# Kernel tuning notes

Hardware: AMD Instinct MI355X
Metric: run time of the kernel (lower is better)

The kernel has to match this reference:

```python
import jax, jax.numpy as jnp
import numpy as np

EPS = 0.0  # GINConv eps

def _gin_conv(x, edge_index, W1, b1, W2, b2, n_nodes):
    # GINConv: mlp((1+eps)*x + sum_{j in N(i)} x_j)
    src, dst = edge_index[0], edge_index[1]
    agg = jax.ops.segment_sum(x[src], dst, num_segments=n_nodes)  # [N, d]
    h = (1.0 + EPS) * x + agg
    h = jax.nn.relu(h @ W1 + b1)  # Linear -> Identity(BN off) -> ReLU
    return h @ W2 + b2            # second Linear


def setup_inputs() -> dict:
    key = jax.random.key(0)
    ks = jax.random.split(key, 10)
    N, E = 50000, 600000
    d_in, d_hid, d_out = 128, 256, 128
    x = jax.random.normal(ks[0], (N, d_in), dtype=jnp.float32)
    edge_index = jax.random.randint(ks[1], (2, E), 0, N, dtype=jnp.int64)

    def lin(k, fan_in, fan_out):
        bound = 1.0 / np.sqrt(fan_in)
        kw, kb = jax.random.split(k)
        W = jax.random.uniform(kw, (fan_in, fan_out), jnp.float32, -bound, bound)
        b = jax.random.uniform(kb, (fan_out,), jnp.float32, -bound, bound)
        return W, b

    W1a, b1a = lin(ks[2], d_in, d_hid)   # conv0 mlp: 128->256
    W2a, b2a = lin(ks[3], d_hid, d_hid)  # conv0 mlp: 256->256
    W1b, b1b = lin(ks[4], d_hid, d_hid)  # conv1 mlp: 256->256
    W2b, b2b = lin(ks[5], d_hid, d_out)  # conv1 mlp: 256->128
    return {"x": x, "W1a": W1a, "b1a": b1a, "W2a": W2a, "b2a": b2a,
            "W1b": W1b, "b1b": b1b, "W2b": W2b, "b2b": b2b,
            "edge_index": edge_index}


def reference(x, W1a, b1a, W2a, b2a, W1b, b1b, W2b, b2b, edge_index):
    n_nodes = x.shape[0]
    # layer 0: GINConv -> relu (use_bn=False; dropout is identity in eval)
    h = _gin_conv(x, edge_index, W1a, b1a, W2a, b2a, n_nodes)
    h = jax.nn.relu(h)
    # final GINConv (no activation after, per forward())
    return _gin_conv(h, edge_index, W1b, b1b, W2b, b2b, n_nodes)
```

## Files before the change

kernel.cpp:

```cpp
#include <hip/hip_runtime.h>


typedef __bf16 bf16x8 __attribute__((ext_vector_type(8)));
typedef float f32x4 __attribute__((ext_vector_type(4)));
typedef unsigned short u16x8 __attribute__((ext_vector_type(8)));
typedef unsigned short u16x4 __attribute__((ext_vector_type(4)));
typedef unsigned int uint32;

__device__ __forceinline__ unsigned short f2bf(float f) {
  uint32 u = __builtin_bit_cast(uint32, f);
  u += 0x7FFFu + ((u >> 16) & 1u);
  return (unsigned short)(u >> 16);
}
__device__ __forceinline__ float bf2f(unsigned short h) {
  return __builtin_bit_cast(float, (uint32)h << 16);
}

#define G2L16(gp, lp)                                                        \
  __builtin_amdgcn_global_load_lds(                                          \
      (const __attribute__((address_space(1))) void*)(gp),                   \
      (__attribute__((address_space(3))) void*)(lp), 16, 0, 0)

__global__ void hist(const int* __restrict__ eidx, int* __restrict__ deg, int E) {
  int e = blockIdx.x * blockDim.x + threadIdx.x;
  if (e < E) atomicAdd(&deg[eidx[e + E]], 1);
}

__global__ __launch_bounds__(256) void block_sums(const int* __restrict__ deg,
                                                  int* __restrict__ bsum, int Nn) {
  __shared__ int sm[256];
  int t = threadIdx.x;
  int i = blockIdx.x * 256 + t;
  sm[t] = (i < Nn) ? deg[i] : 0;
  __syncthreads();
#pragma unroll
  for (int off = 128; off > 0; off >>= 1) {
    if (t < off) sm[t] += sm[t + off];
    __syncthreads();
  }
  if (t == 0) bsum[blockIdx.x] = sm[0];
}

__global__ __launch_bounds__(256) void scan_bsums(int* __restrict__ bsum, int nb) {
  __shared__ int sm[256];
  int t = threadIdx.x;
  int v = (t < nb) ? bsum[t] : 0;
  sm[t] = v;
  __syncthreads();
#pragma unroll
  for (int off = 1; off < 256; off <<= 1) {
    int add = (t >= off) ? sm[t - off] : 0;
    __syncthreads();
    sm[t] += add;
    __syncthreads();
  }
  if (t < nb) bsum[t] = sm[t] - v;
}

__global__ __launch_bounds__(256) void block_scan(const int* __restrict__ deg,
                                                  const int* __restrict__ bsum,
                                                  int* __restrict__ offs,
                                                  int* __restrict__ pos, int Nn) {
  __shared__ int sm[256];
  int t = threadIdx.x;
  int i = blockIdx.x * 256 + t;
  int v = (i < Nn) ? deg[i] : 0;
  sm[t] = v;
  __syncthreads();
#pragma unroll
  for (int off = 1; off < 256; off <<= 1) {
    int add = (t >= off) ? sm[t - off] : 0;
    __syncthreads();
    sm[t] += add;
    __syncthreads();
  }
  int ex = bsum[blockIdx.x] + sm[t] - v;
  if (i < Nn) {
    offs[i] = ex;
    pos[i] = ex;
    if (i == Nn - 1) offs[Nn] = ex + v;
  }
}

__global__ void fill_csr(const int* __restrict__ eidx, int* __restrict__ pos,
                         int* __restrict__ esrc, int E) {
  int e = blockIdx.x * blockDim.x + threadIdx.x;
  if (e < E) {
    int s = eidx[e];
    int d = eidx[e + E];
    int p = atomicAdd(&pos[d], 1);
    esrc[p] = s;
  }
}

__global__ __launch_bounds__(256) void prep(
    int* __restrict__ deg, int Nn,
    const float* __restrict__ x, unsigned short* __restrict__ xb, long long n4,
    const float* __restrict__ W1a, const float* __restrict__ W2a,
    const float* __restrict__ W1b, const float* __restrict__ W2b,
    unsigned short* __restrict__ w1t, unsigned short* __restrict__ w2t,
    unsigned short* __restrict__ w3t, unsigned short* __restrict__ w4t) {
  int zb = (Nn + 255) >> 8;
  int b = blockIdx.x;
  int t = threadIdx.x;
  if (b < zb) {
    int i = b * 256 + t;
    if (i < Nn) deg[i] = 0;
  } else if (b < zb + 768) {
    int i = (b - zb) * 256 + t;
    const float* W;
    unsigned short* WT;
    int K, N, j;
    if (i < 32768) {
      W = W1a; WT = w1t; K = 128; N = 256; j = i;
    } else if (i < 98304) {
      W = W2a; WT = w2t; K = 256; N = 256; j = i - 32768;
    } else if (i < 163840) {
      W = W1b; WT = w3t; K = 256; N = 256; j = i - 98304;
    } else {
      W = W2b; WT = w4t; K = 256; N = 128; j = i - 163840;
    }
    int k = j / N, n = j - k * N;
    WT[n * K + k] = f2bf(W[j]);
  } else {
    long long i = (long long)(b - zb - 768) * 256 + t;
    long long stride = (long long)(gridDim.x - zb - 768) * 256;
    for (; i < n4; i += stride) {
      float4 v = ((const float4*)x)[i];
      u16x4 o;
      o.x = f2bf(v.x); o.y = f2bf(v.y); o.z = f2bf(v.z); o.w = f2bf(v.w);
      ((u16x4*)xb)[i] = o;
    }
  }
}

__global__ __launch_bounds__(256) void agg_bf16_128(
    unsigned short* __restrict__ out, const unsigned short* __restrict__ xb,
    const int* __restrict__ offs, const int* __restrict__ esrc, int Nn) {
  int node = blockIdx.x * 4 + (threadIdx.x >> 6);
  if (node >= Nn) return;
  int lane = threadIdx.x & 63;
  int sub = lane >> 4, l16 = lane & 15;
  int beg = offs[node], end = offs[node + 1];
  int total = end - beg + 1;
  const unsigned short* xp = xb + l16 * 8;
  float acc[8] = {};
  for (int j0 = 0; j0 < total; j0 += 16) {
#pragma unroll
    for (int u = 0; u < 4; ++u) {
      int j = j0 + u * 4 + sub;
      int rv = esrc[beg + j - (j > 0)];
      long long row = (j > 0 && j < total) ? rv : node;
      float sel = (j < total) ? 1.f : 0.f;
      u16x8 v = *(const u16x8*)(xp + row * 128);
#pragma unroll
      for (int k = 0; k < 8; ++k)
        acc[k] = fmaf(bf2f(v[k]), sel, acc[k]);
    }
  }
#pragma unroll
  for (int k = 0; k < 8; ++k) acc[k] += __shfl_xor(acc[k], 16);
#pragma unroll
  for (int k = 0; k < 8; ++k) acc[k] += __shfl_xor(acc[k], 32);
  if (sub == 0) {
    u16x8 o;
#pragma unroll
    for (int k = 0; k < 8; ++k) o[k] = f2bf(acc[k]);
    *(u16x8*)(out + (long long)node * 128 + l16 * 8) = o;
  }
}

__global__ __launch_bounds__(256) void agg_bf16_256(
    unsigned short* __restrict__ out, const unsigned short* __restrict__ h,
    const int* __restrict__ offs, const int* __restrict__ esrc, int Nn) {
  int node = blockIdx.x * 4 + (threadIdx.x >> 6);
  if (node >= Nn) return;
  int lane = threadIdx.x & 63;
  int sub = lane >> 5, l32 = lane & 31;
  int beg = offs[node], end = offs[node + 1];
  int total = end - beg + 1;
  const unsigned short* hp = h + l32 * 8;
  float acc[8] = {};
  for (int j0 = 0; j0 < total; j0 += 16) {
#pragma unroll
    for (int u = 0; u < 8; ++u) {
      int j = j0 + u * 2 + sub;
      int rv = esrc[beg + j - (j > 0)];
      long long row = (j > 0 && j < total) ? rv : node;
      float sel = (j < total) ? 1.f : 0.f;
      u16x8 v = *(const u16x8*)(hp + row * 256);
#pragma unroll
      for (int k = 0; k < 8; ++k)
        acc[k] = fmaf(bf2f(v[k]), sel, acc[k]);
    }
  }
#pragma unroll
  for (int k = 0; k < 8; ++k) acc[k] += __shfl_xor(acc[k], 32);
  if (sub == 0) {
    u16x8 o;
#pragma unroll
    for (int k = 0; k < 8; ++k) o[k] = f2bf(acc[k]);
    *(u16x8*)(out + (long long)node * 256 + l32 * 8) = o;
  }
}

template <int K1, int N2, bool OUT_BF16>
__global__ __launch_bounds__(256) void fused_mlp(
    const unsigned short* __restrict__ A,
    const unsigned short* __restrict__ BT1, const float* __restrict__ b1,
    const unsigned short* __restrict__ BT2, const float* __restrict__ b2,
    void* __restrict__ Cout, int M) {
  __shared__ unsigned short As[64 * 32];
  __shared__ unsigned short Bs[256 * 32];
  __shared__ unsigned short Ts[64 * 264];
  const int tid = threadIdx.x;
  const int wave = tid >> 6, lane = tid & 63;
  const int quad = lane >> 4, l16 = lane & 15;
  const int rowBase = blockIdx.x * 64;
  const int r16 = lane >> 2;
  const int kq = lane & 3;

  long long arow = min(rowBase + wave * 16 + r16, M - 1);
  const unsigned short* ga = A + arow * K1 + kq * 8;
  const unsigned short* gb = BT1 + (long long)(wave * 64 + r16) * K1 + kq * 8;
  unsigned short* la = As + wave * 16 * 32;
  f32x4 acc[4][4] = {};
  for (int k0 = 0; k0 < K1; k0 += 32) {
    G2L16(ga, la);
    ga += 32;
#pragma unroll
    for (int c = 0; c < 4; ++c)
      G2L16(gb + (long long)(16 * c) * K1, Bs + (wave * 64 + 16 * c) * 32);
    gb += 32;
    __syncthreads();
    bf16x8 af[4], bfr[4];
#pragma unroll
    for (int mi = 0; mi < 4; ++mi)
      af[mi] = *(const bf16x8*)(As + (mi * 16 + l16) * 32 + quad * 8);
#pragma unroll
    for (int ni = 0; ni < 4; ++ni)
      bfr[ni] = *(const bf16x8*)(Bs + (wave * 64 + ni * 16 + l16) * 32 + quad * 8);
#pragma unroll
    for (int mi = 0; mi < 4; ++mi)
#pragma unroll
      for (int ni = 0; ni < 4; ++ni)
        acc[mi][ni] = __builtin_amdgcn_mfma_f32_16x16x32_bf16(
            af[mi], bfr[ni], acc[mi][ni], 0, 0, 0);
    __syncthreads();
  }
#pragma unroll
  for (int ni = 0; ni < 4; ++ni) {
    int col = wave * 64 + ni * 16 + l16;
    float bv = b1[col];
#pragma unroll
    for (int mi = 0; mi < 4; ++mi)
#pragma unroll
      for (int r = 0; r < 4; ++r) {
        int row = mi * 16 + quad * 4 + r;
        Ts[row * 264 + col] = f2bf(fmaxf(acc[mi][ni][r] + bv, 0.f));
      }
  }
  __syncthreads();

  constexpr int NI2 = N2 / 64;
  const int wcol = wave * (N2 / 4);
  const unsigned short* gb2 = BT2 + (long long)(wcol + r16) * 256 + kq * 8;
  f32x4 acc2[4][NI2] = {};
  for (int k2 = 0; k2 < 256; k2 += 32) {
#pragma unroll
    for (int c = 0; c < NI2; ++c)
      G2L16(gb2 + (long long)(16 * c) * 256, Bs + (wcol + 16 * c) * 32);
    gb2 += 32;
    __syncthreads();
    bf16x8 af[4], bfr[NI2];
#pragma unroll
    for (int mi = 0; mi < 4; ++mi)
      af[mi] = *(const bf16x8*)(Ts + (mi * 16 + l16) * 264 + k2 + quad * 8);
#pragma unroll
    for (int ni = 0; ni < NI2; ++ni)
      bfr[ni] = *(const bf16x8*)(Bs + (wcol + ni * 16 + l16) * 32 + quad * 8);
#pragma unroll
    for (int mi = 0; mi < 4; ++mi)
#pragma unroll
      for (int ni = 0; ni < NI2; ++ni)
        acc2[mi][ni] = __builtin_amdgcn_mfma_f32_16x16x32_bf16(
            af[mi], bfr[ni], acc2[mi][ni], 0, 0, 0);
    __syncthreads();
  }
#pragma unroll
  for (int ni = 0; ni < NI2; ++ni) {
    int col = wcol + ni * 16 + l16;
    float bv = b2[col];
#pragma unroll
    for (int mi = 0; mi < 4; ++mi)
#pragma unroll
      for (int r = 0; r < 4; ++r) {
        int row = rowBase + mi * 16 + quad * 4 + r;
        if (row < M) {
          float o = acc2[mi][ni][r] + bv;
          if (OUT_BF16)
            ((unsigned short*)Cout)[(long long)row * N2 + col] = f2bf(fmaxf(o, 0.f));
          else
            ((float*)Cout)[(long long)row * N2 + col] = o;
        }
      }
  }
}

extern "C" void kernel_launch(void* const* d_in, const int* in_sizes, int n_in,
                              void* d_out, int out_size, void* d_ws, size_t ws_size,
                              hipStream_t stream) {
  const float* x   = (const float*)d_in[0];
  const float* W1a = (const float*)d_in[1];
  const float* b1a = (const float*)d_in[2];
  const float* W2a = (const float*)d_in[3];
  const float* b2a = (const float*)d_in[4];
  const float* W1b = (const float*)d_in[5];
  const float* b1b = (const float*)d_in[6];
  const float* W2b = (const float*)d_in[7];
  const float* b2b = (const float*)d_in[8];
  const int*   ei  = (const int*)d_in[9];

  const int Nn = in_sizes[0] / 128;
  const int E  = in_sizes[9] / 2;
  float* out = (float*)d_out;

  unsigned short* h   = (unsigned short*)d_ws;
  unsigned short* g0  = h  + (size_t)Nn * 256;
  unsigned short* g1  = g0 + (size_t)Nn * 128;
  unsigned short* xb  = g1 + (size_t)Nn * 256;
  unsigned short* w1t = xb + (size_t)Nn * 128;
  unsigned short* w2t = w1t + 256 * 128;
  unsigned short* w3t = w2t + 256 * 256;
  unsigned short* w4t = w3t + 256 * 256;
  int* deg  = (int*)(w4t + 128 * 256);
  int* offs = deg + Nn;
  int* pos  = offs + Nn + 1;
  int* esrc = pos + Nn;
  int* bsum = esrc + E;

  dim3 blk(256);
  int nb = (Nn + 255) / 256;

  prep<<<nb + 768 + 2048, blk, 0, stream>>>(deg, Nn, x, xb,
                                            (long long)Nn * 128 / 4,
                                            W1a, W2a, W1b, W2b,
                                            w1t, w2t, w3t, w4t);
  hist<<<(E + 255) / 256, blk, 0, stream>>>(ei, deg, E);
  block_sums<<<nb, blk, 0, stream>>>(deg, bsum, Nn);
  scan_bsums<<<1, blk, 0, stream>>>(bsum, nb);
  block_scan<<<nb, blk, 0, stream>>>(deg, bsum, offs, pos, Nn);
  fill_csr<<<(E + 255) / 256, blk, 0, stream>>>(ei, pos, esrc, E);

  int aggBlocks = (Nn + 3) / 4;
  int mlpBlocks = (Nn + 63) / 64;

  agg_bf16_128<<<aggBlocks, blk, 0, stream>>>(g0, xb, offs, esrc, Nn);
  fused_mlp<128, 256, true><<<mlpBlocks, blk, 0, stream>>>(
      g0, w1t, b1a, w2t, b2a, h, Nn);

  agg_bf16_256<<<aggBlocks, blk, 0, stream>>>(g1, h, offs, esrc, Nn);
  fused_mlp<256, 128, false><<<mlpBlocks, blk, 0, stream>>>(
      g1, w3t, b1b, w4t, b2b, out, Nn);
}
```

Baseline: 294.0 us.

## Fuse neighbor aggregation into the MLP kernel via shared-memory staging

Each GIN layer's gather-sum aggregation now runs inside the fused MLP kernel. Every wave aggregates 16 nodes into a shared-memory tile, and the first GEMM reads that tile directly instead of loading an intermediate buffer from global memory. This removes the g0/g1 round-trip through global memory and two kernel launches. In exchange, each block runs aggregation for its 64 rows serially (16 nodes per wave) with fewer blocks in flight, which may reduce how well gather latency is hidden compared with the separate 4-nodes-per-block agg kernels.

After: 328.6 us. +11.7%, slower.

```diff
diff --git a/kernel.cpp b/kernel.cpp
--- a/kernel.cpp
+++ b/kernel.cpp
@@ -134,109 +134,102 @@
   }
 }
 
-__global__ __launch_bounds__(256) void agg_bf16_128(
-    unsigned short* __restrict__ out, const unsigned short* __restrict__ xb,
-    const int* __restrict__ offs, const int* __restrict__ esrc, int Nn) {
-  int node = blockIdx.x * 4 + (threadIdx.x >> 6);
-  if (node >= Nn) return;
-  int lane = threadIdx.x & 63;
-  int sub = lane >> 4, l16 = lane & 15;
-  int beg = offs[node], end = offs[node + 1];
-  int total = end - beg + 1;
-  const unsigned short* xp = xb + l16 * 8;
-  float acc[8] = {};
-  for (int j0 = 0; j0 < total; j0 += 16) {
-#pragma unroll
-    for (int u = 0; u < 4; ++u) {
-      int j = j0 + u * 4 + sub;
-      int rv = esrc[beg + j - (j > 0)];
-      long long row = (j > 0 && j < total) ? rv : node;
-      float sel = (j < total) ? 1.f : 0.f;
-      u16x8 v = *(const u16x8*)(xp + row * 128);
-#pragma unroll
-      for (int k = 0; k < 8; ++k)
-        acc[k] = fmaf(bf2f(v[k]), sel, acc[k]);
-    }
-  }
-#pragma unroll
-  for (int k = 0; k < 8; ++k) acc[k] += __shfl_xor(acc[k], 16);
-#pragma unroll
-  for (int k = 0; k < 8; ++k) acc[k] += __shfl_xor(acc[k], 32);
-  if (sub == 0) {
-    u16x8 o;
-#pragma unroll
-    for (int k = 0; k < 8; ++k) o[k] = f2bf(acc[k]);
-    *(u16x8*)(out + (long long)node * 128 + l16 * 8) = o;
-  }
-}
-
-__global__ __launch_bounds__(256) void agg_bf16_256(
-    unsigned short* __restrict__ out, const unsigned short* __restrict__ h,
-    const int* __restrict__ offs, const int* __restrict__ esrc, int Nn) {
-  int node = blockIdx.x * 4 + (threadIdx.x >> 6);
-  if (node >= Nn) return;
-  int lane = threadIdx.x & 63;
-  int sub = lane >> 5, l32 = lane & 31;
-  int beg = offs[node], end = offs[node + 1];
-  int total = end - beg + 1;
-  const unsigned short* hp = h + l32 * 8;
-  float acc[8] = {};
-  for (int j0 = 0; j0 < total; j0 += 16) {
-#pragma unroll
-    for (int u = 0; u < 8; ++u) {
-      int j = j0 + u * 2 + sub;
-      int rv = esrc[beg + j - (j > 0)];
-      long long row = (j > 0 && j < total) ? rv : node;
-      float sel = (j < total) ? 1.f : 0.f;
-      u16x8 v = *(const u16x8*)(hp + row * 256);
-#pragma unroll
-      for (int k = 0; k < 8; ++k)
-        acc[k] = fmaf(bf2f(v[k]), sel, acc[k]);
-    }
-  }
-#pragma unroll
-  for (int k = 0; k < 8; ++k) acc[k] += __shfl_xor(acc[k], 32);
-  if (sub == 0) {
-    u16x8 o;
-#pragma unroll
-    for (int k = 0; k < 8; ++k) o[k] = f2bf(acc[k]);
-    *(u16x8*)(out + (long long)node * 256 + l32 * 8) = o;
-  }
-}
-
-template <int K1, int N2, bool OUT_BF16>
-__global__ __launch_bounds__(256) void fused_mlp(
-    const unsigned short* __restrict__ A,
+template <int D, int N2, bool OUT_BF16>
+__global__ __launch_bounds__(256) void fused_gin(
+    const unsigned short* __restrict__ X,
+    const int* __restrict__ offs, const int* __restrict__ esrc,
     const unsigned short* __restrict__ BT1, const float* __restrict__ b1,
     const unsigned short* __restrict__ BT2, const float* __restrict__ b2,
     void* __restrict__ Cout, int M) {
-  __shared__ unsigned short As[64 * 32];
+  constexpr int LDT = 264;
+  constexpr int LDX = (D == 128) ? 136 : 264;
+  __shared__ unsigned short Ts[64 * LDT];
   __shared__ unsigned short Bs[256 * 32];
-  __shared__ unsigned short Ts[64 * 264];
+  unsigned short* Xs = Ts;
   const int tid = threadIdx.x;
   const int wave = tid >> 6, lane = tid & 63;
   const int quad = lane >> 4, l16 = lane & 15;
   const int rowBase = blockIdx.x * 64;
+
+  if (D == 128) {
+    int grp = lane >> 4;
+    int l = lane & 15;
+    const unsigned short* xp = X + l * 8;
+    for (int i = 0; i < 16; ++i) {
+      int cn = min(rowBase + wave * 16 + i, M - 1);
+      int beg = offs[cn], end = offs[cn + 1];
+      int total = end - beg + 1;
+      float acc[8] = {};
+      for (int j0 = 0; j0 < total; j0 += 16) {
+#pragma unroll
+        for (int u = 0; u < 4; ++u) {
+          int j = j0 + u * 4 + grp;
+          int rv = esrc[beg + j - (j > 0)];
+          long long row = (j > 0 && j < total) ? rv : cn;
+          float sel = (j < total) ? 1.f : 0.f;
+          u16x8 v = *(const u16x8*)(xp + row * D);
+#pragma unroll
+          for (int k = 0; k < 8; ++k) acc[k] = fmaf(bf2f(v[k]), sel, acc[k]);
+        }
+      }
+#pragma unroll
+      for (int k = 0; k < 8; ++k) acc[k] += __shfl_xor(acc[k], 16);
+#pragma unroll
+      for (int k = 0; k < 8; ++k) acc[k] += __shfl_xor(acc[k], 32);
+      if (grp == 0) {
+        u16x8 o;
+#pragma unroll
+        for (int k = 0; k < 8; ++k) o[k] = f2bf(acc[k]);
+        *(u16x8*)(Xs + (wave * 16 + i) * LDX + l * 8) = o;
+      }
+    }
+  } else {
+    int grp = lane >> 5;
+    int l = lane & 31;
+    const unsigned short* xp = X + l * 8;
+    for (int i = 0; i < 16; ++i) {
+      int cn = min(rowBase + wave * 16 + i, M - 1);
+      int beg = offs[cn], end = offs[cn + 1];
+      int total = end - beg + 1;
+      float acc[8] = {};
+      for (int j0 = 0; j0 < total; j0 += 16) {
+#pragma unroll
+        for (int u = 0; u < 8; ++u) {
+          int j = j0 + u * 2 + grp;
+          int rv = esrc[beg + j - (j > 0)];
+          long long row = (j > 0 && j < total) ? rv : cn;
+          float sel = (j < total) ? 1.f : 0.f;
+          u16x8 v = *(const u16x8*)(xp + row * D);
+#pragma unroll
+          for (int k = 0; k < 8; ++k) acc[k] = fmaf(bf2f(v[k]), sel, acc[k]);
+        }
+      }
+#pragma unroll
+      for (int k = 0; k < 8; ++k) acc[k] += __shfl_xor(acc[k], 32);
+      if (grp == 0) {
+        u16x8 o;
+#pragma unroll
+        for (int k = 0; k < 8; ++k) o[k] = f2bf(acc[k]);
+        *(u16x8*)(Xs + (wave * 16 + i) * LDX + l * 8) = o;
+      }
+    }
+  }
+  __syncthreads();
+
   const int r16 = lane >> 2;
   const int kq = lane & 3;
-
-  long long arow = min(rowBase + wave * 16 + r16, M - 1);
-  const unsigned short* ga = A + arow * K1 + kq * 8;
-  const unsigned short* gb = BT1 + (long long)(wave * 64 + r16) * K1 + kq * 8;
-  unsigned short* la = As + wave * 16 * 32;
-  f32x4 acc[4][4] = {};
-  for (int k0 = 0; k0 < K1; k0 += 32) {
-    G2L16(ga, la);
-    ga += 32;
+  const unsigned short* gb = BT1 + (long long)(wave * 64 + r16) * D + kq * 8;
+  f32x4 acc1[4][4] = {};
+  for (int k0 = 0; k0 < D; k0 += 32) {
 #pragma unroll
     for (int c = 0; c < 4; ++c)
-      G2L16(gb + (long long)(16 * c) * K1, Bs + (wave * 64 + 16 * c) * 32);
+      G2L16(gb + (long long)(16 * c) * D, Bs + (wave * 64 + 16 * c) * 32);
     gb += 32;
     __syncthreads();
     bf16x8 af[4], bfr[4];
 #pragma unroll
     for (int mi = 0; mi < 4; ++mi)
-      af[mi] = *(const bf16x8*)(As + (mi * 16 + l16) * 32 + quad * 8);
+      af[mi] = *(const bf16x8*)(Xs + (mi * 16 + l16) * LDX + k0 + quad * 8);
 #pragma unroll
     for (int ni = 0; ni < 4; ++ni)
       bfr[ni] = *(const bf16x8*)(Bs + (wave * 64 + ni * 16 + l16) * 32 + quad * 8);
@@ -244,8 +237,8 @@
     for (int mi = 0; mi < 4; ++mi)
 #pragma unroll
       for (int ni = 0; ni < 4; ++ni)
-        acc[mi][ni] = __builtin_amdgcn_mfma_f32_16x16x32_bf16(
-            af[mi], bfr[ni], acc[mi][ni], 0, 0, 0);
+        acc1[mi][ni] = __builtin_amdgcn_mfma_f32_16x16x32_bf16(
+            af[mi], bfr[ni], acc1[mi][ni], 0, 0, 0);
     __syncthreads();
   }
 #pragma unroll
@@ -257,7 +250,7 @@
 #pragma unroll
       for (int r = 0; r < 4; ++r) {
         int row = mi * 16 + quad * 4 + r;
-        Ts[row * 264 + col] = f2bf(fmaxf(acc[mi][ni][r] + bv, 0.f));
+        Ts[row * LDT + col] = f2bf(fmaxf(acc1[mi][ni][r] + bv, 0.f));
       }
   }
   __syncthreads();
@@ -275,7 +268,7 @@
     bf16x8 af[4], bfr[NI2];
 #pragma unroll
     for (int mi = 0; mi < 4; ++mi)
-      af[mi] = *(const bf16x8*)(Ts + (mi * 16 + l16) * 264 + k2 + quad * 8);
+      af[mi] = *(const bf16x8*)(Ts + (mi * 16 + l16) * LDT + k2 + quad * 8);
 #pragma unroll
     for (int ni = 0; ni < NI2; ++ni)
       bfr[ni] = *(const bf16x8*)(Bs + (wcol + ni * 16 + l16) * 32 + quad * 8);
@@ -326,9 +319,7 @@
   float* out = (float*)d_out;
 
   unsigned short* h   = (unsigned short*)d_ws;
-  unsigned short* g0  = h  + (size_t)Nn * 256;
-  unsigned short* g1  = g0 + (size_t)Nn * 128;
-  unsigned short* xb  = g1 + (size_t)Nn * 256;
+  unsigned short* xb  = h  + (size_t)Nn * 256;
   unsigned short* w1t = xb + (size_t)Nn * 128;
   unsigned short* w2t = w1t + 256 * 128;
   unsigned short* w3t = w2t + 256 * 256;
@@ -352,14 +343,10 @@
   block_scan<<<nb, blk, 0, stream>>>(deg, bsum, offs, pos, Nn);
   fill_csr<<<(E + 255) / 256, blk, 0, stream>>>(ei, pos, esrc, E);
 
-  int aggBlocks = (Nn + 3) / 4;
-  int mlpBlocks = (Nn + 63) / 64;
-
-  agg_bf16_128<<<aggBlocks, blk, 0, stream>>>(g0, xb, offs, esrc, Nn);
-  fused_mlp<128, 256, true><<<mlpBlocks, blk, 0, stream>>>(
-      g0, w1t, b1a, w2t, b2a, h, Nn);
-
-  agg_bf16_256<<<aggBlocks, blk, 0, stream>>>(g1, h, offs, esrc, Nn);
-  fused_mlp<256, 128, false><<<mlpBlocks, blk, 0, stream>>>(
-      g1, w3t, b1b, w4t, b2b, out, Nn);
-}
+  int gb = (Nn + 63) / 64;
+
+  fused_gin<128, 256, true><<<gb, blk, 0, stream>>>(
+      xb, offs, esrc, w1t, b1a, w2t, b2a, h, Nn);
+  fused_gin<256, 128, false><<<gb, blk, 0, stream>>>(
+      h, offs, esrc, w3t, b1b, w4t, b2b, out, Nn);
+}
```

## Fuse three-kernel degree scan into single-pass scan and pack bf16 accumulation

Applied to the files above, without the earlier changes.

Replaces the block_sums/scan_bsums/block_scan kernel chain with one scan kernel. Every block publishes its aggregate through global flags, block 0 scans the aggregates, and the other blocks spin until that prefix is ready. This removes two kernel launches and their gaps. The aggregation kernels now decode bf16 pairs from 32-bit words and accumulate in float2 vectors, which may map to packed FMA instructions. The spin-wait depends on all 196 blocks being co-resident and on the flag array being zeroed by prep, which is now extended to cover it.

Measured after the change: 293.5 us. About the same (-0.2%).

```diff
diff --git a/kernel.cpp b/kernel.cpp
--- a/kernel.cpp
+++ b/kernel.cpp
@@ -3,17 +3,22 @@
 
 typedef __bf16 bf16x8 __attribute__((ext_vector_type(8)));
 typedef float f32x4 __attribute__((ext_vector_type(4)));
+typedef float f32x2 __attribute__((ext_vector_type(2)));
+typedef unsigned short u16x4 __attribute__((ext_vector_type(4)));
 typedef unsigned short u16x8 __attribute__((ext_vector_type(8)));
-typedef unsigned short u16x4 __attribute__((ext_vector_type(4)));
 typedef unsigned int uint32;
+typedef uint32 u32x4 __attribute__((ext_vector_type(4)));
 
 __device__ __forceinline__ unsigned short f2bf(float f) {
   uint32 u = __builtin_bit_cast(uint32, f);
   u += 0x7FFFu + ((u >> 16) & 1u);
   return (unsigned short)(u >> 16);
 }
-__device__ __forceinline__ float bf2f(unsigned short h) {
-  return __builtin_bit_cast(float, (uint32)h << 16);
+__device__ __forceinline__ f32x2 bfpair(uint32 w) {
+  f32x2 r;
+  r.x = __builtin_bit_cast(float, w << 16);
+  r.y = __builtin_bit_cast(float, w & 0xFFFF0000u);
+  return r;
 }
 
 #define G2L16(gp, lp)                                                        \
@@ -26,44 +31,15 @@
   if (e < E) atomicAdd(&deg[eidx[e + E]], 1);
 }
 
-__global__ __launch_bounds__(256) void block_sums(const int* __restrict__ deg,
-                                                  int* __restrict__ bsum, int Nn) {
+__global__ __launch_bounds__(256) void scan_all(
+    const int* __restrict__ deg, int* __restrict__ offs, int* __restrict__ pos,
+    int* __restrict__ aggr, int* __restrict__ incl, int* __restrict__ flg,
+    int Nn, int nb) {
   __shared__ int sm[256];
-  int t = threadIdx.x;
-  int i = blockIdx.x * 256 + t;
-  sm[t] = (i < Nn) ? deg[i] : 0;
-  __syncthreads();
-#pragma unroll
-  for (int off = 128; off > 0; off >>= 1) {
-    if (t < off) sm[t] += sm[t + off];
-    __syncthreads();
-  }
-  if (t == 0) bsum[blockIdx.x] = sm[0];
-}
-
-__global__ __launch_bounds__(256) void scan_bsums(int* __restrict__ bsum, int nb) {
-  __shared__ int sm[256];
-  int t = threadIdx.x;
-  int v = (t < nb) ? bsum[t] : 0;
-  sm[t] = v;
-  __syncthreads();
-#pragma unroll
-  for (int off = 1; off < 256; off <<= 1) {
-    int add = (t >= off) ? sm[t - off] : 0;
-    __syncthreads();
-    sm[t] += add;
-    __syncthreads();
-  }
-  if (t < nb) bsum[t] = sm[t] - v;
-}
-
-__global__ __launch_bounds__(256) void block_scan(const int* __restrict__ deg,
-                                                  const int* __restrict__ bsum,
-                                                  int* __restrict__ offs,
-                                                  int* __restrict__ pos, int Nn) {
-  __shared__ int sm[256];
-  int t = threadIdx.x;
-  int i = blockIdx.x * 256 + t;
+  __shared__ int s_prefix;
+  const int t = threadIdx.x;
+  const int b = blockIdx.x;
+  const int i = b * 256 + t;
   int v = (i < Nn) ? deg[i] : 0;
   sm[t] = v;
   __syncthreads();
@@ -74,7 +50,37 @@
     sm[t] += add;
     __syncthreads();
   }
-  int ex = bsum[blockIdx.x] + sm[t] - v;
+  if (t == 255) {
+    atomicExch(&aggr[b], sm[255]);
+    atomicExch(&flg[b], 1);
+  }
+  if (b == 0) {
+    for (int j = t; j < nb; j += 256)
+      while (atomicAdd(&flg[j], 0) == 0) __builtin_amdgcn_s_sleep(1);
+    __syncthreads();
+    int a = (t < nb) ? atomicAdd(&aggr[t], 0) : 0;
+    __shared__ int sb[256];
+    sb[t] = a;
+    __syncthreads();
+#pragma unroll
+    for (int off = 1; off < 256; off <<= 1) {
+      int add = (t >= off) ? sb[t - off] : 0;
+      __syncthreads();
+      sb[t] += add;
+      __syncthreads();
+    }
+    if (t < nb) atomicExch(&incl[t], sb[t]);
+    __syncthreads();
+    if (t == 0) atomicExch(&flg[nb], 1);
+    if (t == 0) s_prefix = 0;
+  } else {
+    if (t == 0) {
+      while (atomicAdd(&flg[nb], 0) == 0) __builtin_amdgcn_s_sleep(8);
+      s_prefix = atomicAdd(&incl[b - 1], 0);
+    }
+  }
+  __syncthreads();
+  int ex = s_prefix + sm[t] - v;
   if (i < Nn) {
     offs[i] = ex;
     pos[i] = ex;
@@ -94,18 +100,18 @@
 }
 
 __global__ __launch_bounds__(256) void prep(
-    int* __restrict__ deg, int Nn,
+    int* __restrict__ zp, int zn,
     const float* __restrict__ x, unsigned short* __restrict__ xb, long long n4,
     const float* __restrict__ W1a, const float* __restrict__ W2a,
     const float* __restrict__ W1b, const float* __restrict__ W2b,
     unsigned short* __restrict__ w1t, unsigned short* __restrict__ w2t,
     unsigned short* __restrict__ w3t, unsigned short* __restrict__ w4t) {
-  int zb = (Nn + 255) >> 8;
+  int zb = (zn + 255) >> 8;
   int b = blockIdx.x;
   int t = threadIdx.x;
   if (b < zb) {
     int i = b * 256 + t;
-    if (i < Nn) deg[i] = 0;
+    if (i < zn) zp[i] = 0;
   } else if (b < zb + 768) {
     int i = (b - zb) * 256 + t;
     const float* W;
@@ -140,32 +146,35 @@
   int node = blockIdx.x * 4 + (threadIdx.x >> 6);
   if (node >= Nn) return;
   int lane = threadIdx.x & 63;
-  int sub = lane >> 4, l16 = lane & 15;
+  int grp = lane >> 4, l16 = lane & 15;
   int beg = offs[node], end = offs[node + 1];
   int total = end - beg + 1;
   const unsigned short* xp = xb + l16 * 8;
-  float acc[8] = {};
+  f32x2 acc[4] = {};
   for (int j0 = 0; j0 < total; j0 += 16) {
 #pragma unroll
     for (int u = 0; u < 4; ++u) {
-      int j = j0 + u * 4 + sub;
+      int j = j0 + u * 4 + grp;
       int rv = esrc[beg + j - (j > 0)];
       long long row = (j > 0 && j < total) ? rv : node;
       float sel = (j < total) ? 1.f : 0.f;
-      u16x8 v = *(const u16x8*)(xp + row * 128);
-#pragma unroll
-      for (int k = 0; k < 8; ++k)
-        acc[k] = fmaf(bf2f(v[k]), sel, acc[k]);
-    }
-  }
-#pragma unroll
-  for (int k = 0; k < 8; ++k) acc[k] += __shfl_xor(acc[k], 16);
-#pragma unroll
-  for (int k = 0; k < 8; ++k) acc[k] += __shfl_xor(acc[k], 32);
-  if (sub == 0) {
+      f32x2 fsel = {sel, sel};
+      u32x4 w = *(const u32x4*)(xp + row * 128);
+#pragma unroll
+      for (int k = 0; k < 4; ++k) acc[k] += bfpair(w[k]) * fsel;
+    }
+  }
+  float s[8];
+#pragma unroll
+  for (int k = 0; k < 4; ++k) { s[2 * k] = acc[k].x; s[2 * k + 1] = acc[k].y; }
+#pragma unroll
+  for (int k = 0; k < 8; ++k) s[k] += __shfl_xor(s[k], 16);
+#pragma unroll
+  for (int k = 0; k < 8; ++k) s[k] += __shfl_xor(s[k], 32);
+  if (grp == 0) {
     u16x8 o;
 #pragma unroll
-    for (int k = 0; k < 8; ++k) o[k] = f2bf(acc[k]);
+    for (int k = 0; k < 8; ++k) o[k] = f2bf(s[k]);
     *(u16x8*)(out + (long long)node * 128 + l16 * 8) = o;
   }
 }
@@ -176,30 +185,33 @@
   int node = blockIdx.x * 4 + (threadIdx.x >> 6);
   if (node >= Nn) return;
   int lane = threadIdx.x & 63;
-  int sub = lane >> 5, l32 = lane & 31;
+  int grp = lane >> 5, l32 = lane & 31;
   int beg = offs[node], end = offs[node + 1];
   int total = end - beg + 1;
   const unsigned short* hp = h + l32 * 8;
-  float acc[8] = {};
+  f32x2 acc[4] = {};
   for (int j0 = 0; j0 < total; j0 += 16) {
 #pragma unroll
     for (int u = 0; u < 8; ++u) {
-      int j = j0 + u * 2 + sub;
+      int j = j0 + u * 2 + grp;
       int rv = esrc[beg + j - (j > 0)];
       long long row = (j > 0 && j < total) ? rv : node;
       float sel = (j < total) ? 1.f : 0.f;
-      u16x8 v = *(const u16x8*)(hp + row * 256);
-#pragma unroll
-      for (int k = 0; k < 8; ++k)
-        acc[k] = fmaf(bf2f(v[k]), sel, acc[k]);
-    }
-  }
-#pragma unroll
-  for (int k = 0; k < 8; ++k) acc[k] += __shfl_xor(acc[k], 32);
-  if (sub == 0) {
+      f32x2 fsel = {sel, sel};
+      u32x4 w = *(const u32x4*)(hp + row * 256);
+#pragma unroll
+      for (int k = 0; k < 4; ++k) acc[k] += bfpair(w[k]) * fsel;
+    }
+  }
+  float s[8];
+#pragma unroll
+  for (int k = 0; k < 4; ++k) { s[2 * k] = acc[k].x; s[2 * k + 1] = acc[k].y; }
+#pragma unroll
+  for (int k = 0; k < 8; ++k) s[k] += __shfl_xor(s[k], 32);
+  if (grp == 0) {
     u16x8 o;
 #pragma unroll
-    for (int k = 0; k < 8; ++k) o[k] = f2bf(acc[k]);
+    for (int k = 0; k < 8; ++k) o[k] = f2bf(s[k]);
     *(u16x8*)(out + (long long)node * 256 + l32 * 8) = o;
   }
 }
@@ -325,6 +337,8 @@
   const int E  = in_sizes[9] / 2;
   float* out = (float*)d_out;
 
+  const int nb = (Nn + 255) / 256;
+
   unsigned short* h   = (unsigned short*)d_ws;
   unsigned short* g0  = h  + (size_t)Nn * 256;
   unsigned short* g1  = g0 + (size_t)Nn * 128;
@@ -334,22 +348,23 @@
   unsigned short* w3t = w2t + 256 * 256;
   unsigned short* w4t = w3t + 256 * 256;
   int* deg  = (int*)(w4t + 128 * 256);
-  int* offs = deg + Nn;
+  int* flg  = deg + Nn;
+  int* aggr = flg + nb + 1;
+  int* incl = aggr + nb;
+  int* offs = incl + nb;
   int* pos  = offs + Nn + 1;
   int* esrc = pos + Nn;
-  int* bsum = esrc + E;
 
   dim3 blk(256);
-  int nb = (Nn + 255) / 256;
-
-  prep<<<nb + 768 + 2048, blk, 0, stream>>>(deg, Nn, x, xb,
+  int zn = Nn + nb + 1;
+  int zb = (zn + 255) / 256;
+
+  prep<<<zb + 768 + 2048, blk, 0, stream>>>(deg, zn, x, xb,
                                             (long long)Nn * 128 / 4,
                                             W1a, W2a, W1b, W2b,
                                             w1t, w2t, w3t, w4t);
   hist<<<(E + 255) / 256, blk, 0, stream>>>(ei, deg, E);
-  block_sums<<<nb, blk, 0, stream>>>(deg, bsum, Nn);
-  scan_bsums<<<1, blk, 0, stream>>>(bsum, nb);
-  block_scan<<<nb, blk, 0, stream>>>(deg, bsum, offs, pos, Nn);
+  scan_all<<<nb, blk, 0, stream>>>(deg, offs, pos, aggr, incl, flg, Nn, nb);
   fill_csr<<<(E + 255) / 256, blk, 0, stream>>>(ei, pos, esrc, E);
 
   int aggBlocks = (Nn + 3) / 4;
@@ -358,7 +373,6 @@
   agg_bf16_128<<<aggBlocks, blk, 0, stream>>>(g0, xb, offs, esrc, Nn);
   fused_mlp<128, 256, true><<<mlpBlocks, blk, 0, stream>>>(
       g0, w1t, b1a, w2t, b2a, h, Nn);
-
   agg_bf16_256<<<aggBlocks, blk, 0, stream>>>(g1, h, offs, esrc, Nn);
   fused_mlp<256, 128, false><<<mlpBlocks, blk, 0, stream>>>(
       g1, w3t, b1b, w4t, b2b, out, Nn);
```
